# Kernel tuning notes

Hardware: AMD Instinct MI355X
Metric: run time of the kernel (lower is better)

Reference implementation:

```python
import jax, jax.numpy as jnp
import numpy as np

NUM_CLASSES = 2   # module init num_classes; class logits have NUM_CLASSES+1 (incl. 'no object')
ORIG_H, ORIG_W = 512, 512  # original input resolution that masks are upsampled to


def setup_inputs() -> dict:
    key = jax.random.key(0)
    k1, k2 = jax.random.split(key)
    B, Q = 8, 100
    h, w = 128, 128  # mask decoder outputs at 1/4 input resolution
    class_queries_logits = jax.random.normal(k1, (B, Q, NUM_CLASSES + 1), dtype=jnp.float32)
    masks_queries_logits = jax.random.normal(k2, (B, Q, h, w), dtype=jnp.float32)
    return {"class_queries_logits": class_queries_logits,
            "masks_queries_logits": masks_queries_logits}


def reference(class_queries_logits, masks_queries_logits):
    B, Q = masks_queries_logits.shape[:2]
    # bilinear upsample to original resolution (align_corners=False == half-pixel centers)
    masks_up = jax.image.resize(masks_queries_logits, (B, Q, ORIG_H, ORIG_W), method="bilinear")
    # softmax over classes (incl. no-object), keep only the first NUM_CLASSES,
    # exactly as the original loop only indexes c in range(num_classes)
    class_probs = jax.nn.softmax(class_queries_logits, axis=-1)[..., :NUM_CLASSES]  # [B,Q,C]
    mask_probs = jax.nn.sigmoid(masks_up)  # [B,Q,H,W]
    # fused replacement for the triple b/q/c Python loop of weighted accumulates
    logits = jnp.einsum("bqc,bqhw->bchw", class_probs, mask_probs)  # [B,C,H,W]
    return logits
```

## Files before the change

### kernel.cpp

```cpp
#include <hip/hip_runtime.h>
#include <math.h>

#define NB 8
#define NQ 100
#define NQH 50
#define NCP1 3
#define NC 2
#define HIN 128
#define WIN 128
#define HOUT 512
#define WOUT 512
#define QSTR (HIN * WIN)
#define QBYTES (QSTR * 4)

#if __has_builtin(__builtin_amdgcn_exp2f)
#define EXP2F(x) __builtin_amdgcn_exp2f(x)
#else
#define EXP2F(x) exp2f(x)
#endif
#if __has_builtin(__builtin_amdgcn_rcpf)
#define RCPF(x) __builtin_amdgcn_rcpf(x)
#else
#define RCPF(x) (1.0f / (x))
#endif

__device__ __forceinline__ float bperm(int byteaddr, float v) {
  return __int_as_float(__builtin_amdgcn_ds_bpermute(byteaddr, __float_as_int(v)));
}

__global__ __launch_bounds__(512, 4)
void m2f_fused(const float* __restrict__ cls,
               const float* __restrict__ masks,
               float* __restrict__ out) {
  const int k   = blockIdx.x;
  const int b   = blockIdx.y;
  const int tid = threadIdx.x;

  __shared__ float2 pq[NQ];
  __shared__ float  part[16][256];

  if (tid < NQ) {
    const float* cl = cls + (b * NQ + tid) * NCP1;
    float a0 = cl[0], a1 = cl[1], a2 = cl[2];
    float mx = fmaxf(a0, fmaxf(a1, a2));
    const float L2E = 1.4426950408889634f;
    float e0 = EXP2F((a0 - mx) * L2E);
    float e1 = EXP2F((a1 - mx) * L2E);
    float e2 = EXP2F((a2 - mx) * L2E);
    float inv = RCPF(e0 + e1 + e2);
    pq[tid] = make_float2(e0 * inv, e1 * inv);
  }
  __syncthreads();

  const int wave = tid >> 6;
  const int r    = wave & 3;
  const int qh   = wave >> 2;
  const int lane = tid & 63;
  const int q0   = qh * NQH;

  const int rlo = (r < 2) ? (k > 0 ? k - 1 : 0) : k;
  const int rhi = (r < 2) ? k : (k < HIN - 1 ? k + 1 : HIN - 1);
  const float NL2E = -1.4426950408889634f;
  const float wlo = ((r == 0) ? 0.375f : (r == 1) ? 0.125f
                   : (r == 2) ? 0.875f : 0.625f) * NL2E;
  const float whi = ((r == 0) ? 0.625f : (r == 1) ? 0.875f
                   : (r == 2) ? 0.125f : 0.375f) * NL2E;

  const int voffA = q0 * QBYTES + (rlo * WIN + 2 * lane) * 4;
  const int voffB = q0 * QBYTES + (rhi * WIN + 2 * lane) * 4;
  const float* const basep = masks + (size_t)b * NQ * QSTR;

  const int addrL = (lane - 1) << 2;
  const int addrR = (lane + 1) << 2;
  const bool edgeL = (lane == 0);
  const bool edgeR = (lane == 63);

  float c0[8], c1[8];
#pragma unroll
  for (int j = 0; j < 8; ++j) { c0[j] = 0.f; c1[j] = 0.f; }

  float2 A0, B0, A1, B1, A2, B2, A3, B3, A4, B4;

#define LOADSET(S, qrel)                                                  \
  do {                                                                    \
    asm volatile("global_load_dwordx2 %0, %2, %3\n\t"                     \
                 "global_load_dwordx2 %1, %4, %3"                         \
                 : "=&v"(A##S), "=&v"(B##S)                               \
                 : "v"(voffA + (qrel) * QBYTES), "s"(basep),              \
                   "v"(voffB + (qrel) * QBYTES));                         \
  } while (0)

#define WAITS(S)                                                          \
  asm volatile("s_waitcnt vmcnt(8)" : "+v"(A##S), "+v"(B##S))

#define COMPUTE(S, qq)                                                    \
  do {                                                                    \
    const float2 pd = pq[qq];                                             \
    float t0 = fmaf(wlo, A##S.x, whi * B##S.x);             \
    float t1 = fmaf(wlo, A##S.y, whi * B##S.y);             \
    float tLr = bperm(addrL, t1);                                         \
    float tL = edgeL ? t0 : tLr;                                          \
    float m01 = 0.5f * (t0 + t1);                                         \
    float mL  = 0.5f * (tL + t0);                                         \
    float s0  = RCPF(1.0f + EXP2F(t0));                                   \
    float s1  = RCPF(1.0f + EXP2F(t1));                                   \
    float sm  = RCPF(1.0f + EXP2F(m01));                                  \
    float sL  = RCPF(1.0f + EXP2F(mL));                                   \
    float sRr = bperm(addrR, sL);                                         \
    float sR  = edgeR ? s1 : sRr;                                         \
    float dL = s0 - sL, d0 = sm - s0, d1 = s1 - sm, dR = sR - s1;         \
    float g0 = fmaf(0.25f, dL, sL);                                       \
    float g1 = fmaf(0.75f, dL, sL);                                       \
    float g2 = fmaf(0.25f, d0, s0);                                       \
    float g3 = fmaf(0.75f, d0, s0);                                       \
    float g4 = fmaf(0.25f, d1, sm);                                       \
    float g5 = fmaf(0.75f, d1, sm);                                       \
    float g6 = fmaf(0.25f, dR, s1);                                       \
    float g7 = fmaf(0.75f, dR, s1);                                       \
    c0[0] = fmaf(pd.x, g0, c0[0]);  c1[0] = fmaf(pd.y, g0, c1[0]);        \
    c0[1] = fmaf(pd.x, g1, c0[1]);  c1[1] = fmaf(pd.y, g1, c1[1]);        \
    c0[2] = fmaf(pd.x, g2, c0[2]);  c1[2] = fmaf(pd.y, g2, c1[2]);        \
    c0[3] = fmaf(pd.x, g3, c0[3]);  c1[3] = fmaf(pd.y, g3, c1[3]);        \
    c0[4] = fmaf(pd.x, g4, c0[4]);  c1[4] = fmaf(pd.y, g4, c1[4]);        \
    c0[5] = fmaf(pd.x, g5, c0[5]);  c1[5] = fmaf(pd.y, g5, c1[5]);        \
    c0[6] = fmaf(pd.x, g6, c0[6]);  c1[6] = fmaf(pd.y, g6, c1[6]);        \
    c0[7] = fmaf(pd.x, g7, c0[7]);  c1[7] = fmaf(pd.y, g7, c1[7]);        \
  } while (0)

  LOADSET(0, 0); LOADSET(1, 1); LOADSET(2, 2); LOADSET(3, 3); LOADSET(4, 4);

  for (int q = 0; q < NQH - 5; q += 5) {
    WAITS(0); COMPUTE(0, q0 + q);     LOADSET(0, q + 5);
    WAITS(1); COMPUTE(1, q0 + q + 1); LOADSET(1, q + 6);
    WAITS(2); COMPUTE(2, q0 + q + 2); LOADSET(2, q + 7);
    WAITS(3); COMPUTE(3, q0 + q + 3); LOADSET(3, q + 8);
    WAITS(4); COMPUTE(4, q0 + q + 4); LOADSET(4, q + 9);
  }

  asm volatile("s_waitcnt vmcnt(0)"
               : "+v"(A0), "+v"(B0), "+v"(A1), "+v"(B1), "+v"(A2), "+v"(B2),
                 "+v"(A3), "+v"(B3), "+v"(A4), "+v"(B4));
  COMPUTE(0, q0 + NQH - 5);
  COMPUTE(1, q0 + NQH - 4);
  COMPUTE(2, q0 + NQH - 3);
  COMPUTE(3, q0 + NQH - 2);
  COMPUTE(4, q0 + NQH - 1);

  const int col = r * 64 + lane;
  if (qh == 1) {
#pragma unroll
    for (int j = 0; j < 8; ++j) { part[j][col] = c0[j]; part[j + 8][col] = c1[j]; }
  }
  __syncthreads();
  if (qh == 0) {
#pragma unroll
    for (int j = 0; j < 8; ++j) { c0[j] += part[j][col]; c1[j] += part[j + 8][col]; }

    const int y  = 4 * k + r;
    const int x0 = 8 * lane;
    float* o0 = out + (((size_t)b * NC + 0) * HOUT + y) * WOUT + x0;
    float* o1 = out + (((size_t)b * NC + 1) * HOUT + y) * WOUT + x0;
    *(float4*)o0       = make_float4(c0[0], c0[1], c0[2], c0[3]);
    *(float4*)(o0 + 4) = make_float4(c0[4], c0[5], c0[6], c0[7]);
    *(float4*)o1       = make_float4(c1[0], c1[1], c1[2], c1[3]);
    *(float4*)(o1 + 4) = make_float4(c1[4], c1[5], c1[6], c1[7]);
  }
}

extern "C" void kernel_launch(void* const* d_in, const int* in_sizes, int n_in,
                              void* d_out, int out_size, void* d_ws, size_t ws_size,
                              hipStream_t stream) {
  const float* cls   = (const float*)d_in[0];
  const float* masks = (const float*)d_in[1];
  float* out = (float*)d_out;
  dim3 grid(HIN, NB);
  m2f_fused<<<grid, 512, 0, stream>>>(cls, masks, out);
}
```

Baseline: 118.0 us.

## Accumulate weighted sigmoid samples before horizontal interpolation instead of after

Horizontal interpolation is linear, so the kernel now accumulates the class-weighted sigmoid values at four intermediate sample positions per lane across queries. The 8-tap horizontal interpolation and the right-neighbor shuffle run once at the end instead of once per query. This removes per-query FMAs and a bpermute from the inner loop and halves the shared-memory partial buffer and accumulator registers. Results change only by floating-point reassociation.

```diff
diff --git a/kernel.cpp b/kernel.cpp
--- a/kernel.cpp
+++ b/kernel.cpp
@@ -37,7 +37,7 @@
   const int tid = threadIdx.x;
 
   __shared__ float2 pq[NQ];
-  __shared__ float  part[16][256];
+  __shared__ float  part[8][256];
 
   if (tid < NQ) {
     const float* cl = cls + (b * NQ + tid) * NCP1;
@@ -75,9 +75,10 @@
   const bool edgeL = (lane == 0);
   const bool edgeR = (lane == 63);
 
-  float c0[8], c1[8];
-#pragma unroll
-  for (int j = 0; j < 8; ++j) { c0[j] = 0.f; c1[j] = 0.f; }
+  float2 aSL = make_float2(0.f, 0.f);
+  float2 aS0 = make_float2(0.f, 0.f);
+  float2 aSM = make_float2(0.f, 0.f);
+  float2 aS1 = make_float2(0.f, 0.f);
 
   float2 A0, B0, A1, B1, A2, B2, A3, B3, A4, B4;
 
@@ -106,25 +107,10 @@
     float s1  = RCPF(1.0f + EXP2F(t1));                                   \
     float sm  = RCPF(1.0f + EXP2F(m01));                                  \
     float sL  = RCPF(1.0f + EXP2F(mL));                                   \
-    float sRr = bperm(addrR, sL);                                         \
-    float sR  = edgeR ? s1 : sRr;                                         \
-    float dL = s0 - sL, d0 = sm - s0, d1 = s1 - sm, dR = sR - s1;         \
-    float g0 = fmaf(0.25f, dL, sL);                                       \
-    float g1 = fmaf(0.75f, dL, sL);                                       \
-    float g2 = fmaf(0.25f, d0, s0);                                       \
-    float g3 = fmaf(0.75f, d0, s0);                                       \
-    float g4 = fmaf(0.25f, d1, sm);                                       \
-    float g5 = fmaf(0.75f, d1, sm);                                       \
-    float g6 = fmaf(0.25f, dR, s1);                                       \
-    float g7 = fmaf(0.75f, dR, s1);                                       \
-    c0[0] = fmaf(pd.x, g0, c0[0]);  c1[0] = fmaf(pd.y, g0, c1[0]);        \
-    c0[1] = fmaf(pd.x, g1, c0[1]);  c1[1] = fmaf(pd.y, g1, c1[1]);        \
-    c0[2] = fmaf(pd.x, g2, c0[2]);  c1[2] = fmaf(pd.y, g2, c1[2]);        \
-    c0[3] = fmaf(pd.x, g3, c0[3]);  c1[3] = fmaf(pd.y, g3, c1[3]);        \
-    c0[4] = fmaf(pd.x, g4, c0[4]);  c1[4] = fmaf(pd.y, g4, c1[4]);        \
-    c0[5] = fmaf(pd.x, g5, c0[5]);  c1[5] = fmaf(pd.y, g5, c1[5]);        \
-    c0[6] = fmaf(pd.x, g6, c0[6]);  c1[6] = fmaf(pd.y, g6, c1[6]);        \
-    c0[7] = fmaf(pd.x, g7, c0[7]);  c1[7] = fmaf(pd.y, g7, c1[7]);        \
+    aSL.x = fmaf(pd.x, sL, aSL.x);  aSL.y = fmaf(pd.y, sL, aSL.y);        \
+    aS0.x = fmaf(pd.x, s0, aS0.x);  aS0.y = fmaf(pd.y, s0, aS0.y);        \
+    aSM.x = fmaf(pd.x, sm, aSM.x);  aSM.y = fmaf(pd.y, sm, aSM.y);        \
+    aS1.x = fmaf(pd.x, s1, aS1.x);  aS1.y = fmaf(pd.y, s1, aS1.y);        \
   } while (0)
 
   LOADSET(0, 0); LOADSET(1, 1); LOADSET(2, 2); LOADSET(3, 3); LOADSET(4, 4);
@@ -148,22 +134,48 @@
 
   const int col = r * 64 + lane;
   if (qh == 1) {
-#pragma unroll
-    for (int j = 0; j < 8; ++j) { part[j][col] = c0[j]; part[j + 8][col] = c1[j]; }
+    part[0][col] = aSL.x;  part[1][col] = aSL.y;
+    part[2][col] = aS0.x;  part[3][col] = aS0.y;
+    part[4][col] = aSM.x;  part[5][col] = aSM.y;
+    part[6][col] = aS1.x;  part[7][col] = aS1.y;
   }
   __syncthreads();
   if (qh == 0) {
-#pragma unroll
-    for (int j = 0; j < 8; ++j) { c0[j] += part[j][col]; c1[j] += part[j + 8][col]; }
+    aSL.x += part[0][col];  aSL.y += part[1][col];
+    aS0.x += part[2][col];  aS0.y += part[3][col];
+    aSM.x += part[4][col];  aSM.y += part[5][col];
+    aS1.x += part[6][col];  aS1.y += part[7][col];
+
+    float SRx_r = bperm(addrR, aSL.x);
+    float SRy_r = bperm(addrR, aSL.y);
+    float SRx = edgeR ? aS1.x : SRx_r;
+    float SRy = edgeR ? aS1.y : SRy_r;
+
+    float o0x = fmaf(0.25f, aS0.x, 0.75f * aSL.x);
+    float o1x = fmaf(0.75f, aS0.x, 0.25f * aSL.x);
+    float o2x = fmaf(0.25f, aSM.x, 0.75f * aS0.x);
+    float o3x = fmaf(0.75f, aSM.x, 0.25f * aS0.x);
+    float o4x = fmaf(0.25f, aS1.x, 0.75f * aSM.x);
+    float o5x = fmaf(0.75f, aS1.x, 0.25f * aSM.x);
+    float o6x = fmaf(0.25f, SRx,   0.75f * aS1.x);
+    float o7x = fmaf(0.75f, SRx,   0.25f * aS1.x);
+    float o0y = fmaf(0.25f, aS0.y, 0.75f * aSL.y);
+    float o1y = fmaf(0.75f, aS0.y, 0.25f * aSL.y);
+    float o2y = fmaf(0.25f, aSM.y, 0.75f * aS0.y);
+    float o3y = fmaf(0.75f, aSM.y, 0.25f * aS0.y);
+    float o4y = fmaf(0.25f, aS1.y, 0.75f * aSM.y);
+    float o5y = fmaf(0.75f, aS1.y, 0.25f * aSM.y);
+    float o6y = fmaf(0.25f, SRy,   0.75f * aS1.y);
+    float o7y = fmaf(0.75f, SRy,   0.25f * aS1.y);
 
     const int y  = 4 * k + r;
     const int x0 = 8 * lane;
     float* o0 = out + (((size_t)b * NC + 0) * HOUT + y) * WOUT + x0;
     float* o1 = out + (((size_t)b * NC + 1) * HOUT + y) * WOUT + x0;
-    *(float4*)o0       = make_float4(c0[0], c0[1], c0[2], c0[3]);
-    *(float4*)(o0 + 4) = make_float4(c0[4], c0[5], c0[6], c0[7]);
-    *(float4*)o1       = make_float4(c1[0], c1[1], c1[2], c1[3]);
-    *(float4*)(o1 + 4) = make_float4(c1[4], c1[5], c1[6], c1[7]);
+    *(float4*)o0       = make_float4(o0x, o1x, o2x, o3x);
+    *(float4*)(o0 + 4) = make_float4(o4x, o5x, o6x, o7x);
+    *(float4*)o1       = make_float4(o0y, o1y, o2y, o3y);
+    *(float4*)(o1 + 4) = make_float4(o4y, o5y, o6y, o7y);
   }
 }
 
```

Result: faster. 111.5 us (-5.5%).
